# Kernel tuning notes

Measured on AMD Instinct MI355X. Metric: run time of the kernel, lower is better.

## Reference

```python
import jax, jax.numpy as jnp
import numpy as np

DIM = 768
NH = 12
HID = int(DIM * 1.5)  # 1152
B_, T_, W_ = 8, 8, 14
HW = 14 * 14
N = HW + 1
BT = B_ * T_


def _ln(x, g, b, eps=1e-5):
    m = jnp.mean(x, axis=-1, keepdims=True)
    v = jnp.var(x, axis=-1, keepdims=True)
    return (x - m) / jnp.sqrt(v + eps) * g + b


def _attn(x, wqkv, wproj, bproj, nh):
    # manual q@k^T -> softmax -> @v, as in the torch module (no qkv bias)
    b, n, c = x.shape
    hd = c // nh
    scale = hd ** -0.5
    qkv = (x @ wqkv.T).reshape(b, n, 3, nh, hd).transpose(2, 0, 3, 1, 4)
    q, k, v = qkv[0], qkv[1], qkv[2]
    a = jax.nn.softmax(jnp.einsum('bhnd,bhmd->bhnm', q, k) * scale, axis=-1)
    o = jnp.einsum('bhnm,bhmd->bhnd', a, v).transpose(0, 2, 1, 3).reshape(b, n, c)
    return o @ wproj.T + bproj


def setup_inputs() -> dict:
    key = jax.random.key(0)
    ks = jax.random.split(key, 16)
    s = 0.02
    d = {
        'x': jax.random.normal(ks[0], (BT, N, DIM), jnp.float32),
        'ln1_g': jnp.ones((DIM,), jnp.float32),
        'ln1_b': jnp.zeros((DIM,), jnp.float32),
        'qkv_w': jax.random.normal(ks[1], (3 * DIM, DIM), jnp.float32) * s,
        'proj_w': jax.random.normal(ks[2], (DIM, DIM), jnp.float32) * s,
        'proj_b': jnp.zeros((DIM,), jnp.float32),
        'tln_g': jnp.ones((DIM,), jnp.float32),
        'tln_b': jnp.zeros((DIM,), jnp.float32),
        'tqkv_w': jax.random.normal(ks[3], (3 * DIM, DIM), jnp.float32) * s,
        'tproj_w': jax.random.normal(ks[4], (DIM, DIM), jnp.float32) * s,
        'tproj_b': jnp.zeros((DIM,), jnp.float32),
        # module zero-inits temporal_fc; use small random so the branch is exercised
        'tfc_w': jax.random.normal(ks[5], (DIM, DIM), jnp.float32) * s,
        'tfc_b': jnp.zeros((DIM,), jnp.float32),
        'ln2_g': jnp.ones((DIM,), jnp.float32),
        'ln2_b': jnp.zeros((DIM,), jnp.float32),
        'fc1_w': jax.random.normal(ks[6], (HID, DIM), jnp.float32) * s,
        'fc1_b': jnp.zeros((HID,), jnp.float32),
        'fc2_w': jax.random.normal(ks[7], (DIM, HID), jnp.float32) * s,
        'fc2_b': jnp.zeros((DIM,), jnp.float32),
        'B': B_, 'T': T_, 'W': W_,
    }
    return d


def reference(x, ln1_g, ln1_b, qkv_w, proj_w, proj_b,
              tln_g, tln_b, tqkv_w, tproj_w, tproj_b, tfc_w, tfc_b,
              ln2_g, ln2_b, fc1_w, fc1_b, fc2_w, fc2_b, B, T, W):
    bt, n, c = x.shape
    hw = n - 1  # spatial tokens (cls excluded)
    # temporal branch: (b t) hw m -> (b hw) t m
    xt = x[:, 1:, :].reshape(B, T, hw, c).transpose(0, 2, 1, 3).reshape(B * hw, T, c)
    xt = _attn(_ln(xt, tln_g, tln_b), tqkv_w, tproj_w, tproj_b, NH)
    xt = xt.reshape(B, hw, T, c).transpose(0, 2, 1, 3).reshape(bt, hw, c)
    xt = xt @ tfc_w.T + tfc_b
    x = x.at[:, 1:, :].add(xt)  # in-place += in torch
    # spatial attention + residual
    x = x + _attn(_ln(x, ln1_g, ln1_b), qkv_w, proj_w, proj_b, NH)
    # MLP + residual (exact GELU, matching nn.GELU default)
    h = jax.nn.gelu(_ln(x, ln2_g, ln2_b) @ fc1_w.T + fc1_b, approximate=False)
    x = x + (h @ fc2_w.T + fc2_b)
    return x
```

## Files before the change

### kernel.cpp

```cpp
#include <hip/hip_runtime.h>
#include <hip/hip_bf16.h>


#define DIM   768
#define NH    12
#define HD    64
#define HID   1152
#define HIDP  1280
#define B_    8
#define T_    8
#define HW_   196
#define NTOK  197
#define BT_   64
#define MROWS (BT_ * NTOK)
#define TROWS (B_ * HW_ * T_)

typedef __bf16 bf16x8 __attribute__((ext_vector_type(8)));
typedef float  f32x4  __attribute__((ext_vector_type(4)));

__device__ inline float bf2f(ushort u) { return __uint_as_float(((unsigned)u) << 16); }
__device__ inline ushort f2bf(float f) {
    unsigned u = __float_as_uint(f);
    unsigned r = (u + 0x7fffu + ((u >> 16) & 1u)) >> 16;
    return (ushort)r;
}

__device__ inline float wred_sum(float v) {
    #pragma unroll
    for (int m = 32; m; m >>= 1) v += __shfl_xor(v, m);
    return v;
}

__device__ __forceinline__ void gload_lds16(const void* g, void* l) {
    __builtin_amdgcn_global_load_lds(
        (const __attribute__((address_space(1))) unsigned int*)g,
        (__attribute__((address_space(3))) unsigned int*)l, 16, 0, 0);
}

__device__ __forceinline__ int xcd_lin(int gid, int nwg) {
    int q = nwg >> 3, r = nwg & 7;
    int xcd = gid & 7, idx = gid >> 3;
    return (xcd < r ? xcd * (q + 1) : r * (q + 1) + (xcd - r) * q) + idx;
}

#define MFMA16(a, b, c) __builtin_amdgcn_mfma_f32_16x16x32_bf16(a, b, c, 0, 0, 0)

__global__ __launch_bounds__(256) void cast_all(
    const float* s0, ushort* d0, int c0, const float* s1, ushort* d1, int c1,
    const float* s2, ushort* d2, int c2, const float* s3, ushort* d3, int c3,
    const float* s4, ushort* d4, int c4)
{
    int i = blockIdx.x * 256 + threadIdx.x;
    const float* s; ushort* d; int base;
    if      (i < c0) { s = s0; d = d0; base = 0;  }
    else if (i < c1) { s = s1; d = d1; base = c0; }
    else if (i < c2) { s = s2; d = d2; base = c1; }
    else if (i < c3) { s = s3; d = d3; base = c2; }
    else if (i < c4) { s = s4; d = d4; base = c3; }
    else return;
    int k = i - base;
    float4 a = *(const float4*)(s + (size_t)k * 8);
    float4 b = *(const float4*)(s + (size_t)k * 8 + 4);
    ushort o[8] = {f2bf(a.x), f2bf(a.y), f2bf(a.z), f2bf(a.w),
                   f2bf(b.x), f2bf(b.y), f2bf(b.z), f2bf(b.w)};
    *(uint4*)(d + (size_t)k * 8) = *(const uint4*)o;
}

__global__ __launch_bounds__(256) void transpose_cast(const float* __restrict__ in, ushort* __restrict__ out)
{
    __shared__ float t[32][33];
    int bx = blockIdx.x % 24, by = blockIdx.x / 24;
    int lx = threadIdx.x & 31, ly = threadIdx.x >> 5;
    #pragma unroll
    for (int i = 0; i < 32; i += 8)
        t[ly + i][lx] = in[(size_t)(by * 32 + ly + i) * DIM + bx * 32 + lx];
    __syncthreads();
    #pragma unroll
    for (int i = 0; i < 32; i += 8)
        out[(size_t)(bx * 32 + ly + i) * DIM + by * 32 + lx] = f2bf(t[lx][ly + i]);
}

__global__ __launch_bounds__(256) void cast_pad_fc2(const float* __restrict__ in, ushort* __restrict__ out)
{
    int i = blockIdx.x * 256 + threadIdx.x;
    if (i >= DIM * (HIDP / 8)) return;
    int r = i / (HIDP / 8), c8 = (i % (HIDP / 8)) * 8;
    ushort o[8];
    if (c8 < HID) {
        const float* s = in + (size_t)r * HID + c8;
        #pragma unroll
        for (int e = 0; e < 8; ++e) o[e] = f2bf(s[e]);
    } else {
        #pragma unroll
        for (int e = 0; e < 8; ++e) o[e] = 0;
    }
    *(uint4*)(out + (size_t)r * HIDP + c8) = *(const uint4*)o;
}

__global__ __launch_bounds__(256) void pad_bias(const float* __restrict__ in, float* __restrict__ out)
{
    int i = blockIdx.x * 256 + threadIdx.x;
    if (i < HIDP) out[i] = (i < HID) ? in[i] : 0.f;
}

__global__ __launch_bounds__(256) void bias_comb(
    const float* __restrict__ tfc_w, const float* __restrict__ tproj_b,
    const float* __restrict__ tfc_b, float* __restrict__ bc)
{
    int w = blockIdx.x * 4 + (threadIdx.x >> 6);
    int lane = threadIdx.x & 63;
    float s = 0.f;
    for (int j = lane; j < DIM; j += 64) s += tfc_w[(size_t)w * DIM + j] * tproj_b[j];
    s = wred_sum(s);
    if (lane == 0) bc[w] = s + tfc_b[w];
}

__global__ __launch_bounds__(256) void init_cls(const float* __restrict__ x, float* __restrict__ out)
{
    int i = blockIdx.x * 256 + threadIdx.x;
    int r = i / 192, c = (i % 192) * 4;
    size_t off = ((size_t)r * NTOK) * DIM + c;
    *(float4*)(out + off) = *(const float4*)(x + off);
}

enum { EPI_STORE = 0, EPI_BIAS_GELU = 1, EPI_BIAS_ADD = 2, EPI_INIT_TFC = 3 };

template <int KK, int EPI>
__global__ __launch_bounds__(512, 1) void gemm256(
    const ushort* __restrict__ Ag, const ushort* __restrict__ Wg,
    const float* __restrict__ bias, ushort* __restrict__ Cg,
    const float* __restrict__ xsrc, float* __restrict__ xf,
    int M, int N, int nm, int nn, int grp)
{
    __shared__ ushort As[2][256 * 64];
    __shared__ ushort Bs[2][256 * 64];

    const int tid  = threadIdx.x;
    const int lane = tid & 63, wid = tid >> 6;
    const int wr = wid >> 2, wc = wid & 3;
    const int fr = lane & 15, fq = lane >> 4;

    int lin = xcd_lin(blockIdx.x, nm * nn);
    int per = grp * nn;
    int g2 = lin / per, rem = lin % per;
    int bm = g2 * grp;
    int gm = nm - bm; if (gm > grp) gm = grp;
    const int m0 = (bm + rem % gm) * 256;
    const int n0 = (rem / gm) * 256;

    const int srow = wid * 8 + (lane >> 3);
    const int scol = 8 * ((lane & 7) ^ (lane >> 3));
    const ushort* aP[4]; const ushort* bP[4];
    #pragma unroll
    for (int j = 0; j < 4; ++j) {
        int ra = m0 + j * 64 + srow; if (ra >= M) ra = M - 1;
        aP[j] = Ag + (size_t)ra * KK + scol;
        bP[j] = Wg + (size_t)(n0 + j * 64 + srow) * KK + scol;
    }
    const int ldso = (wid * 8) * 64;

    f32x4 acc[8][4] = {};
    bf16x8 af[4][2], b0[2][2], b1[2][2];

    const int sw0 = (fq * 8) ^ ((fr & 7) * 8);
    const int sw1 = (32 + fq * 8) ^ ((fr & 7) * 8);

    #pragma unroll
    for (int j = 0; j < 4; ++j) gload_lds16(aP[j], &As[0][j * 4096 + ldso]);
    #pragma unroll
    for (int j = 0; j < 4; ++j) gload_lds16(bP[j], &Bs[0][j * 4096 + ldso]);

    constexpr int NT = KK / 64;
    #pragma unroll
    for (int t = 0; t < NT; ++t) {
        const int rb = t & 1, wb = rb ^ 1;
        const bool st = (t + 1 < NT);
        const int kw = (t + 1) * 64;

        asm volatile("s_waitcnt vmcnt(0)" ::: "memory");
        __builtin_amdgcn_s_barrier();
        __builtin_amdgcn_sched_barrier(0);

        #pragma unroll
        for (int mf = 0; mf < 4; ++mf) {
            af[mf][0] = *(const bf16x8*)&As[rb][(wr * 128 + mf * 16 + fr) * 64 + sw0];
            af[mf][1] = *(const bf16x8*)&As[rb][(wr * 128 + mf * 16 + fr) * 64 + sw1];
        }
        #pragma unroll
        for (int nf = 0; nf < 2; ++nf) {
            b0[nf][0] = *(const bf16x8*)&Bs[rb][(wc * 64 + nf * 16 + fr) * 64 + sw0];
            b0[nf][1] = *(const bf16x8*)&Bs[rb][(wc * 64 + nf * 16 + fr) * 64 + sw1];
        }
        if (st) {
            #pragma unroll
            for (int j = 0; j < 4; ++j) gload_lds16(aP[j] + kw, &As[wb][j * 4096 + ldso]);
        }
        asm volatile("s_waitcnt lgkmcnt(0)" ::: "memory");
        __builtin_amdgcn_sched_barrier(0);
        __builtin_amdgcn_s_setprio(1);
        #pragma unroll
        for (int mf = 0; mf < 4; ++mf)
            #pragma unroll
            for (int nf = 0; nf < 2; ++nf) {
                acc[mf][nf] = MFMA16(af[mf][0], b0[nf][0], acc[mf][nf]);
                acc[mf][nf] = MFMA16(af[mf][1], b0[nf][1], acc[mf][nf]);
            }
        __builtin_amdgcn_s_setprio(0);
        __builtin_amdgcn_sched_barrier(0);

        #pragma unroll
        for (int nf = 0; nf < 2; ++nf) {
            b1[nf][0] = *(const bf16x8*)&Bs[rb][(wc * 64 + (nf + 2) * 16 + fr) * 64 + sw0];
            b1[nf][1] = *(const bf16x8*)&Bs[rb][(wc * 64 + (nf + 2) * 16 + fr) * 64 + sw1];
        }
        if (st) {
            #pragma unroll
            for (int j = 0; j < 4; ++j) gload_lds16(bP[j] + kw, &Bs[wb][j * 4096 + ldso]);
        }
        asm volatile("s_waitcnt lgkmcnt(0)" ::: "memory");
        __builtin_amdgcn_sched_barrier(0);
        __builtin_amdgcn_s_setprio(1);
        #pragma unroll
        for (int mf = 0; mf < 4; ++mf)
            #pragma unroll
            for (int nf = 0; nf < 2; ++nf) {
                acc[mf][nf + 2] = MFMA16(af[mf][0], b1[nf][0], acc[mf][nf + 2]);
                acc[mf][nf + 2] = MFMA16(af[mf][1], b1[nf][1], acc[mf][nf + 2]);
            }
        __builtin_amdgcn_s_setprio(0);
        __builtin_amdgcn_sched_barrier(0);

        #pragma unroll
        for (int mf = 0; mf < 4; ++mf) {
            af[mf][0] = *(const bf16x8*)&As[rb][(wr * 128 + 64 + mf * 16 + fr) * 64 + sw0];
            af[mf][1] = *(const bf16x8*)&As[rb][(wr * 128 + 64 + mf * 16 + fr) * 64 + sw1];
        }
        asm volatile("s_waitcnt lgkmcnt(0)" ::: "memory");
        __builtin_amdgcn_sched_barrier(0);
        __builtin_amdgcn_s_setprio(1);
        #pragma unroll
        for (int mf = 0; mf < 4; ++mf)
            #pragma unroll
            for (int nf = 0; nf < 2; ++nf) {
                acc[mf + 4][nf] = MFMA16(af[mf][0], b0[nf][0], acc[mf + 4][nf]);
                acc[mf + 4][nf] = MFMA16(af[mf][1], b0[nf][1], acc[mf + 4][nf]);
            }
        __builtin_amdgcn_s_setprio(0);
        __builtin_amdgcn_sched_barrier(0);

        __builtin_amdgcn_s_setprio(1);
        #pragma unroll
        for (int mf = 0; mf < 4; ++mf)
            #pragma unroll
            for (int nf = 0; nf < 2; ++nf) {
                acc[mf + 4][nf + 2] = MFMA16(af[mf][0], b1[nf][0], acc[mf + 4][nf + 2]);
                acc[mf + 4][nf + 2] = MFMA16(af[mf][1], b1[nf][1], acc[mf + 4][nf + 2]);
            }
        __builtin_amdgcn_s_setprio(0);
        __builtin_amdgcn_sched_barrier(0);
    }

    #pragma unroll
    for (int mf = 0; mf < 8; ++mf)
        #pragma unroll
        for (int e = 0; e < 4; ++e) {
            int row = m0 + wr * 128 + mf * 16 + fq * 4 + e;
            if (row >= M) continue;
            size_t dstrow = 0;
            if constexpr (EPI == EPI_INIT_TFC) {
                int t2 = row & 7, pp = (row >> 3) % HW_, bb = row / (HW_ * T_);
                dstrow = ((size_t)(bb * T_ + t2) * NTOK + 1 + pp) * DIM;
            }
            #pragma unroll
            for (int nf = 0; nf < 4; ++nf) {
                int col = n0 + wc * 64 + nf * 16 + fr;
                float v = acc[mf][nf][e];
                if constexpr (EPI != EPI_STORE) v += bias[col];
                if constexpr (EPI == EPI_BIAS_GELU) v = 0.5f * v * (1.0f + erff(v * 0.70710678118654752f));
                if constexpr (EPI == EPI_STORE || EPI == EPI_BIAS_GELU) {
                    Cg[(size_t)row * N + col] = f2bf(v);
                } else if constexpr (EPI == EPI_BIAS_ADD) {
                    xf[(size_t)row * DIM + col] += v;
                } else {
                    xf[dstrow + col] = xsrc[dstrow + col] + v;
                }
            }
        }
}

__global__ __launch_bounds__(256) void ln_f32(
    const float* __restrict__ src, const float* __restrict__ g,
    const float* __restrict__ b, ushort* __restrict__ dst, int rows)
{
    int widx = threadIdx.x >> 6, lane = threadIdx.x & 63;
    int r = blockIdx.x * 4 + widx;
    if (r >= rows) return;
    const float* row = src + (size_t)r * DIM;
    float v[12], sum = 0.f, sq = 0.f;
    #pragma unroll
    for (int c = 0; c < 3; ++c) {
        float4 t = *(const float4*)(row + c * 256 + lane * 4);
        v[c*4+0] = t.x; v[c*4+1] = t.y; v[c*4+2] = t.z; v[c*4+3] = t.w;
        sum += t.x + t.y + t.z + t.w;
        sq  += t.x*t.x + t.y*t.y + t.z*t.z + t.w*t.w;
    }
    sum = wred_sum(sum); sq = wred_sum(sq);
    float mean = sum * (1.f / DIM);
    float var  = sq * (1.f / DIM) - mean * mean;
    float rstd = rsqrtf(var + 1e-5f);
    #pragma unroll
    for (int c = 0; c < 3; ++c) {
        int idx = c * 256 + lane * 4;
        float4 gg = *(const float4*)(g + idx);
        float4 bb = *(const float4*)(b + idx);
        ushort4 o;
        o.x = f2bf((v[c*4+0] - mean) * rstd * gg.x + bb.x);
        o.y = f2bf((v[c*4+1] - mean) * rstd * gg.y + bb.y);
        o.z = f2bf((v[c*4+2] - mean) * rstd * gg.z + bb.z);
        o.w = f2bf((v[c*4+3] - mean) * rstd * gg.w + bb.w);
        *(ushort4*)(dst + (size_t)r * DIM + idx) = o;
    }
}

__global__ __launch_bounds__(256) void ln_gather(
    const float* __restrict__ x, const float* __restrict__ g,
    const float* __restrict__ b, ushort* __restrict__ dst, int rows)
{
    int widx = threadIdx.x >> 6, lane = threadIdx.x & 63;
    int r = blockIdx.x * 4 + widx;
    if (r >= rows) return;
    int t = r & 7, pp = (r >> 3) % HW_, bb = r / (HW_ * T_);
    const float* row = x + ((size_t)(bb * T_ + t) * NTOK + 1 + pp) * DIM;
    float v[12], sum = 0.f, sq = 0.f;
    #pragma unroll
    for (int c = 0; c < 3; ++c) {
        float4 t4 = *(const float4*)(row + c * 256 + lane * 4);
        v[c*4+0] = t4.x; v[c*4+1] = t4.y; v[c*4+2] = t4.z; v[c*4+3] = t4.w;
        sum += t4.x + t4.y + t4.z + t4.w;
        sq  += t4.x*t4.x + t4.y*t4.y + t4.z*t4.z + t4.w*t4.w;
    }
    sum = wred_sum(sum); sq = wred_sum(sq);
    float mean = sum * (1.f / DIM);
    float var  = sq * (1.f / DIM) - mean * mean;
    float rstd = rsqrtf(var + 1e-5f);
    #pragma unroll
    for (int c = 0; c < 3; ++c) {
        int idx = c * 256 + lane * 4;
        float4 gg = *(const float4*)(g + idx);
        float4 bb2 = *(const float4*)(b + idx);
        ushort4 o;
        o.x = f2bf((v[c*4+0] - mean) * rstd * gg.x + bb2.x);
        o.y = f2bf((v[c*4+1] - mean) * rstd * gg.y + bb2.y);
        o.z = f2bf((v[c*4+2] - mean) * rstd * gg.z + bb2.z);
        o.w = f2bf((v[c*4+3] - mean) * rstd * gg.w + bb2.w);
        *(ushort4*)(dst + (size_t)r * DIM + idx) = o;
    }
}

__global__ __launch_bounds__(256) void attn_temporal(
    const ushort* __restrict__ qkv, ushort* __restrict__ O)
{
    int widx = threadIdx.x >> 6, lane = threadIdx.x & 63;
    int w = blockIdx.x * 4 + widx;
    int s = w / NH, h = w % NH;
    int qi = lane >> 3, kj = lane & 7;

    const ushort* qrow = qkv + (size_t)(s * 8 + qi) * (3 * DIM) + h * HD;
    const ushort* krow = qkv + (size_t)(s * 8 + kj) * (3 * DIM) + DIM + h * HD;
    float d = 0.f;
    #pragma unroll
    for (int c = 0; c < 8; ++c) {
        uint4 qa = *(const uint4*)(qrow + c * 8);
        uint4 ka = *(const uint4*)(krow + c * 8);
        const ushort* qs = (const ushort*)&qa;
        const ushort* ks = (const ushort*)&ka;
        #pragma unroll
        for (int e = 0; e < 8; ++e) d += bf2f(qs[e]) * bf2f(ks[e]);
    }
    float sc = d * 0.125f;
    float mx = sc;
    #pragma unroll
    for (int m = 4; m; m >>= 1) mx = fmaxf(mx, __shfl_xor(mx, m));
    float p = expf(sc - mx);
    float sum = p;
    #pragma unroll
    for (int m = 4; m; m >>= 1) sum += __shfl_xor(sum, m);
    p /= sum;

    float o[8] = {};
    int base = lane & ~7;
    #pragma unroll
    for (int t = 0; t < 8; ++t) {
        float pt = __shfl(p, base + t);
        const ushort* vrow = qkv + (size_t)(s * 8 + t) * (3 * DIM) + 2 * DIM + h * HD + kj * 8;
        uint4 va = *(const uint4*)vrow;
        const ushort* vs = (const ushort*)&va;
        #pragma unroll
        for (int e = 0; e < 8; ++e) o[e] += pt * bf2f(vs[e]);
    }
    ushort out[8];
    #pragma unroll
    for (int e = 0; e < 8; ++e) out[e] = f2bf(o[e]);
    *(uint4*)(O + (size_t)(s * 8 + qi) * DIM + h * HD + kj * 8) = *(const uint4*)out;
}

#define KS_STRIDE 72
#define VT_STRIDE 208
#define P_STRIDE  208
#define KS_OFF    0
#define VT_OFF    (197 * KS_STRIDE)
#define P_OFF     (VT_OFF + 64 * VT_STRIDE)
#define LDS_TOT   (P_OFF + 4 * 16 * P_STRIDE)

__global__ __launch_bounds__(256, 2) void attn_spatial_mfma(
    const ushort* __restrict__ qkv, ushort* __restrict__ O)
{
    __shared__ ushort lds[LDS_TOT];
    const int tid = threadIdx.x, lane = tid & 63, wid = tid >> 6;
    const int fr = lane & 15, fq = lane >> 4;
    int lin = xcd_lin(blockIdx.x, BT_ * NH);
    const int s = lin / NH, h = lin % NH;
    const size_t base = (size_t)s * NTOK * (3 * DIM);
    const ushort* Qg = qkv + base + h * HD;
    const ushort* Kg = qkv + base + DIM + h * HD;
    const ushort* Vg = qkv + base + 2 * DIM + h * HD;

    for (int chunk = tid; chunk < NTOK * 8; chunk += 256) {
        int r = chunk >> 3, c = (chunk & 7) * 8;
        uint4 v = *(const uint4*)(Kg + (size_t)r * (3 * DIM) + c);
        *(uint4*)&lds[KS_OFF + r * KS_STRIDE + c] = v;
    }
    for (int chunk = tid; chunk < 208 * 8; chunk += 256) {
        int k = chunk >> 3, c = (chunk & 7) * 8;
        uint4 v = {0u, 0u, 0u, 0u};
        if (k < NTOK) v = *(const uint4*)(Vg + (size_t)k * (3 * DIM) + c);
        const ushort* e = (const ushort*)&v;
        #pragma unroll
        for (int j = 0; j < 8; ++j) lds[VT_OFF + (c + j) * VT_STRIDE + k] = e[j];
    }
    __syncthreads();

    ushort* P = &lds[P_OFF + wid * 16 * P_STRIDE];

    for (int qi = wid; qi < 13; qi += 4) {
        int qrow = qi * 16 + fr; if (qrow > NTOK - 1) qrow = NTOK - 1;
        bf16x8 qf0 = *(const bf16x8*)(Qg + (size_t)qrow * (3 * DIM) + fq * 8);
        bf16x8 qf1 = *(const bf16x8*)(Qg + (size_t)qrow * (3 * DIM) + 32 + fq * 8);

        f32x4 sacc[13];
        #pragma unroll
        for (int t = 0; t < 13; ++t) {
            bf16x8 kf0 = *(const bf16x8*)&lds[KS_OFF + (t * 16 + fr) * KS_STRIDE + fq * 8];
            bf16x8 kf1 = *(const bf16x8*)&lds[KS_OFF + (t * 16 + fr) * KS_STRIDE + 32 + fq * 8];
            f32x4 z = {0.f, 0.f, 0.f, 0.f};
            z = MFMA16(kf0, qf0, z);
            sacc[t] = MFMA16(kf1, qf1, z);
        }

        float m = -1e30f;
        #pragma unroll
        for (int t = 0; t < 13; ++t)
            #pragma unroll
            for (int e = 0; e < 4; ++e) {
                int k = t * 16 + fq * 4 + e;
                float v = (k < NTOK) ? sacc[t][e] * 0.125f : -1e30f;
                sacc[t][e] = v;
                m = fmaxf(m, v);
            }
        m = fmaxf(m, __shfl_xor(m, 16));
        m = fmaxf(m, __shfl_xor(m, 32));
        float sum = 0.f;
        #pragma unroll
        for (int t = 0; t < 13; ++t)
            #pragma unroll
            for (int e = 0; e < 4; ++e) {
                float p = expf(sacc[t][e] - m);
                sacc[t][e] = p;
                sum += p;
            }
        sum += __shfl_xor(sum, 16);
        sum += __shfl_xor(sum, 32);
        float rd = 1.f / sum;

        #pragma unroll
        for (int t = 0; t < 13; ++t) {
            ushort2 w0 = { f2bf(sacc[t][0] * rd), f2bf(sacc[t][1] * rd) };
            ushort2 w1 = { f2bf(sacc[t][2] * rd), f2bf(sacc[t][3] * rd) };
            *(ushort2*)&P[fr * P_STRIDE + t * 16 + fq * 4]     = w0;
            *(ushort2*)&P[fr * P_STRIDE + t * 16 + fq * 4 + 2] = w1;
        }

        f32x4 oacc[4] = {};
        #pragma unroll
        for (int st = 0; st < 6; ++st) {
            bf16x8 pf = *(const bf16x8*)&P[fr * P_STRIDE + st * 32 + fq * 8];
            #pragma unroll
            for (int dt = 0; dt < 4; ++dt) {
                bf16x8 vf = *(const bf16x8*)&lds[VT_OFF + (dt * 16 + fr) * VT_STRIDE + st * 32 + fq * 8];
                oacc[dt] = MFMA16(pf, vf, oacc[dt]);
            }
        }
        {
            bf16x8 zz = {};
            bf16x8 pf = zz;
            if (fq < 2) pf = *(const bf16x8*)&P[fr * P_STRIDE + 192 + fq * 8];
            #pragma unroll
            for (int dt = 0; dt < 4; ++dt) {
                bf16x8 vf = zz;
                if (fq < 2) vf = *(const bf16x8*)&lds[VT_OFF + (dt * 16 + fr) * VT_STRIDE + 192 + fq * 8];
                oacc[dt] = MFMA16(pf, vf, oacc[dt]);
            }
        }

        #pragma unroll
        for (int dt = 0; dt < 4; ++dt)
            #pragma unroll
            for (int e = 0; e < 4; ++e) {
                int q = qi * 16 + fq * 4 + e;
                if (q < NTOK)
                    O[(size_t)(s * NTOK + q) * DIM + h * HD + dt * 16 + fr] = f2bf(oacc[dt][e]);
            }
    }
}

extern "C" void kernel_launch(void* const* d_in, const int* in_sizes, int n_in,
                              void* d_out, int out_size, void* d_ws, size_t ws_size,
                              hipStream_t stream)
{
    const float* x      = (const float*)d_in[0];
    const float* ln1_g  = (const float*)d_in[1];
    const float* ln1_b  = (const float*)d_in[2];
    const float* qkv_w  = (const float*)d_in[3];
    const float* proj_w = (const float*)d_in[4];
    const float* proj_b = (const float*)d_in[5];
    const float* tln_g  = (const float*)d_in[6];
    const float* tln_b  = (const float*)d_in[7];
    const float* tqkv_w = (const float*)d_in[8];
    const float* tproj_w= (const float*)d_in[9];
    const float* tproj_b= (const float*)d_in[10];
    const float* tfc_w  = (const float*)d_in[11];
    const float* tfc_b  = (const float*)d_in[12];
    const float* ln2_g  = (const float*)d_in[13];
    const float* ln2_b  = (const float*)d_in[14];
    const float* fc1_w  = (const float*)d_in[15];
    const float* fc1_b  = (const float*)d_in[16];
    const float* fc2_w  = (const float*)d_in[17];
    const float* fc2_b  = (const float*)d_in[18];

    float* out = (float*)d_out;

    char* p = (char*)d_ws;
    ushort* w_qkv  = (ushort*)p; p += (size_t)(3*DIM*DIM) * 2;
    ushort* w_proj = (ushort*)p; p += (size_t)(DIM*DIM) * 2;
    ushort* w_tqkv = (ushort*)p; p += (size_t)(3*DIM*DIM) * 2;
    ushort* w_tfc  = (ushort*)p; p += (size_t)(DIM*DIM) * 2;
    ushort* tprojT = (ushort*)p; p += (size_t)(DIM*DIM) * 2;
    ushort* w_comb = (ushort*)p; p += (size_t)(DIM*DIM) * 2;
    ushort* w_fc1p = (ushort*)p; p += (size_t)(HIDP*DIM) * 2;
    ushort* w_fc2p = (ushort*)p; p += (size_t)(DIM*HIDP) * 2;
    float*  b_comb = (float*)p;  p += DIM * 4;
    float*  fc1_bp = (float*)p;  p += HIDP * 4;
    ushort* bufA   = (ushort*)p; p += (size_t)MROWS * DIM * 2;
    ushort* bufC   = (ushort*)p; p += (size_t)MROWS * DIM * 2;
    ushort* bufB   = (ushort*)p;

    {
        const int DD8 = DIM * DIM / 8;
        int c0 = 3 * DD8;
        int c1 = c0 + DD8;
        int c2 = c1 + 3 * DD8;
        int c3 = c2 + DD8;
        int c4 = c3 + HID * DIM / 8;
        cast_all<<<dim3((c4 + 255) / 256), dim3(256), 0, stream>>>(
            qkv_w, w_qkv, c0, proj_w, w_proj, c1, tqkv_w, w_tqkv, c2,
            tfc_w, w_tfc, c3, fc1_w, w_fc1p, c4);
    }
    hipMemsetAsync(w_fc1p + (size_t)HID * DIM, 0, (size_t)(HIDP - HID) * DIM * 2, stream);
    transpose_cast<<<dim3(576), dim3(256), 0, stream>>>(tproj_w, tprojT);
    cast_pad_fc2<<<dim3((DIM * (HIDP / 8) + 255) / 256), dim3(256), 0, stream>>>(fc2_w, w_fc2p);
    pad_bias<<<dim3((HIDP + 255) / 256), dim3(256), 0, stream>>>(fc1_b, fc1_bp);
    bias_comb<<<dim3(DIM / 4), dim3(256), 0, stream>>>(tfc_w, tproj_b, tfc_b, b_comb);
    init_cls<<<dim3(48), dim3(256), 0, stream>>>(x, out);

    #define GEMM256(KV, EPI, A, W, BIAS, C, XS, XF, M, N, GRP) \
        gemm256<KV, EPI><<<dim3((((M) + 255) / 256) * ((N) / 256)), dim3(512), 0, stream>>>( \
            A, W, BIAS, C, XS, XF, M, N, ((M) + 255) / 256, (N) / 256, GRP)

    GEMM256(DIM, EPI_STORE, w_tfc, tprojT, nullptr, w_comb, nullptr, nullptr, DIM, DIM, 1);

    ln_gather<<<dim3(TROWS / 4), dim3(256), 0, stream>>>(x, tln_g, tln_b, bufA, TROWS);
    GEMM256(DIM, EPI_STORE, bufA, w_tqkv, nullptr, bufB, nullptr, nullptr, TROWS, 3 * DIM, 1);
    attn_temporal<<<dim3(TROWS * NH / 8 / 4), dim3(256), 0, stream>>>(bufB, bufC);
    GEMM256(DIM, EPI_INIT_TFC, bufC, w_comb, b_comb, nullptr, x, out, TROWS, DIM, 1);

    ln_f32<<<dim3((MROWS + 3) / 4), dim3(256), 0, stream>>>(out, ln1_g, ln1_b, bufA, MROWS);
    GEMM256(DIM, EPI_STORE, bufA, w_qkv, nullptr, bufB, nullptr, nullptr, MROWS, 3 * DIM, 1);
    attn_spatial_mfma<<<dim3(BT_ * NH), dim3(256), 0, stream>>>(bufB, bufC);
    GEMM256(DIM, EPI_BIAS_ADD, bufC, w_proj, proj_b, nullptr, nullptr, out, MROWS, DIM, 1);

    ln_f32<<<dim3((MROWS + 3) / 4), dim3(256), 0, stream>>>(out, ln2_g, ln2_b, bufA, MROWS);
    GEMM256(DIM, EPI_BIAS_GELU, bufA, w_fc1p, fc1_bp, bufB, nullptr, nullptr, MROWS, HIDP, 1);
    GEMM256(HIDP, EPI_BIAS_ADD, bufB, w_fc2p, fc2_b, nullptr, nullptr, out, MROWS, DIM, 1);
    #undef GEMM256
}
```

Before: 412.3 us.

## Switch GEMM main loop to triple-buffered BK=32 LDS pipeline

Reworks the 256x256 GEMM K-loop from double-buffered 64-wide K tiles to three LDS slots of 32-wide K tiles with a prefetch distance of two. A partial vmcnt wait replaces the full drain before each barrier. The goal is to keep global loads in flight across iterations and to simplify fragment loading. In exchange there are twice as many barriers per K. The XOR swizzle on the LDS layout is dropped, which risks bank conflicts on the fragment reads.

```diff
diff --git a/kernel.cpp b/kernel.cpp
--- a/kernel.cpp
+++ b/kernel.cpp
@@ -132,8 +132,8 @@
     const float* __restrict__ xsrc, float* __restrict__ xf,
     int M, int N, int nm, int nn, int grp)
 {
-    __shared__ ushort As[2][256 * 64];
-    __shared__ ushort Bs[2][256 * 64];
+    __shared__ ushort As[3][256 * 32];
+    __shared__ ushort Bs[3][256 * 32];
 
     const int tid  = threadIdx.x;
     const int lane = tid & 63, wid = tid >> 6;
@@ -148,114 +148,72 @@
     const int m0 = (bm + rem % gm) * 256;
     const int n0 = (rem / gm) * 256;
 
-    const int srow = wid * 8 + (lane >> 3);
-    const int scol = 8 * ((lane & 7) ^ (lane >> 3));
-    const ushort* aP[4]; const ushort* bP[4];
-    #pragma unroll
-    for (int j = 0; j < 4; ++j) {
-        int ra = m0 + j * 64 + srow; if (ra >= M) ra = M - 1;
+    const int srow = tid >> 2;
+    const int scol = (tid & 3) * 8;
+    const ushort* aP[2]; const ushort* bP[2];
+    #pragma unroll
+    for (int j = 0; j < 2; ++j) {
+        int ra = m0 + j * 128 + srow; if (ra >= M) ra = M - 1;
         aP[j] = Ag + (size_t)ra * KK + scol;
-        bP[j] = Wg + (size_t)(n0 + j * 64 + srow) * KK + scol;
-    }
-    const int ldso = (wid * 8) * 64;
+        bP[j] = Wg + (size_t)(n0 + j * 128 + srow) * KK + scol;
+    }
+    const int ldso = wid * 512;
+
+    auto STAGE_A = [&](int slot, int k0) {
+        gload_lds16(aP[0] + k0, &As[slot][ldso]);
+        gload_lds16(aP[1] + k0, &As[slot][4096 + ldso]);
+    };
+    auto STAGE_B = [&](int slot, int k0) {
+        gload_lds16(bP[0] + k0, &Bs[slot][ldso]);
+        gload_lds16(bP[1] + k0, &Bs[slot][4096 + ldso]);
+    };
 
     f32x4 acc[8][4] = {};
-    bf16x8 af[4][2], b0[2][2], b1[2][2];
-
-    const int sw0 = (fq * 8) ^ ((fr & 7) * 8);
-    const int sw1 = (32 + fq * 8) ^ ((fr & 7) * 8);
-
-    #pragma unroll
-    for (int j = 0; j < 4; ++j) gload_lds16(aP[j], &As[0][j * 4096 + ldso]);
-    #pragma unroll
-    for (int j = 0; j < 4; ++j) gload_lds16(bP[j], &Bs[0][j * 4096 + ldso]);
-
-    constexpr int NT = KK / 64;
+
+    STAGE_A(0, 0);  STAGE_B(0, 0);
+    STAGE_A(1, 32); STAGE_B(1, 32);
+
+    constexpr int NT = KK / 32;
     #pragma unroll
     for (int t = 0; t < NT; ++t) {
-        const int rb = t & 1, wb = rb ^ 1;
-        const bool st = (t + 1 < NT);
-        const int kw = (t + 1) * 64;
-
-        asm volatile("s_waitcnt vmcnt(0)" ::: "memory");
+        const int sl = t % 3, tg = (t + 2) % 3;
+
+        if (t < NT - 1) asm volatile("s_waitcnt vmcnt(4)" ::: "memory");
+        else            asm volatile("s_waitcnt vmcnt(0)" ::: "memory");
         __builtin_amdgcn_s_barrier();
         __builtin_amdgcn_sched_barrier(0);
 
-        #pragma unroll
-        for (int mf = 0; mf < 4; ++mf) {
-            af[mf][0] = *(const bf16x8*)&As[rb][(wr * 128 + mf * 16 + fr) * 64 + sw0];
-            af[mf][1] = *(const bf16x8*)&As[rb][(wr * 128 + mf * 16 + fr) * 64 + sw1];
-        }
-        #pragma unroll
-        for (int nf = 0; nf < 2; ++nf) {
-            b0[nf][0] = *(const bf16x8*)&Bs[rb][(wc * 64 + nf * 16 + fr) * 64 + sw0];
-            b0[nf][1] = *(const bf16x8*)&Bs[rb][(wc * 64 + nf * 16 + fr) * 64 + sw1];
-        }
-        if (st) {
-            #pragma unroll
-            for (int j = 0; j < 4; ++j) gload_lds16(aP[j] + kw, &As[wb][j * 4096 + ldso]);
-        }
+        bf16x8 a0[4], a1[4], b[4];
+        #pragma unroll
+        for (int mf = 0; mf < 4; ++mf)
+            a0[mf] = *(const bf16x8*)&As[sl][(wr * 128 + mf * 16 + fr) * 32 + fq * 8];
+        #pragma unroll
+        for (int nf = 0; nf < 4; ++nf)
+            b[nf] = *(const bf16x8*)&Bs[sl][(wc * 64 + nf * 16 + fr) * 32 + fq * 8];
+        __builtin_amdgcn_sched_barrier(0);
+        #pragma unroll
+        for (int mf = 0; mf < 4; ++mf)
+            a1[mf] = *(const bf16x8*)&As[sl][(wr * 128 + 64 + mf * 16 + fr) * 32 + fq * 8];
+        if (t + 2 < NT) STAGE_A(tg, (t + 2) * 32);
+        asm volatile("s_waitcnt lgkmcnt(4)" ::: "memory");
+        __builtin_amdgcn_sched_barrier(0);
+        __builtin_amdgcn_s_setprio(1);
+        #pragma unroll
+        for (int mf = 0; mf < 4; ++mf)
+            #pragma unroll
+            for (int nf = 0; nf < 4; ++nf)
+                acc[mf][nf] = MFMA16(a0[mf], b[nf], acc[mf][nf]);
+        __builtin_amdgcn_s_setprio(0);
+        __builtin_amdgcn_sched_barrier(0);
+        if (t + 2 < NT) STAGE_B(tg, (t + 2) * 32);
         asm volatile("s_waitcnt lgkmcnt(0)" ::: "memory");
         __builtin_amdgcn_sched_barrier(0);
         __builtin_amdgcn_s_setprio(1);
         #pragma unroll
         for (int mf = 0; mf < 4; ++mf)
             #pragma unroll
-            for (int nf = 0; nf < 2; ++nf) {
-                acc[mf][nf] = MFMA16(af[mf][0], b0[nf][0], acc[mf][nf]);
-                acc[mf][nf] = MFMA16(af[mf][1], b0[nf][1], acc[mf][nf]);
-            }
-        __builtin_amdgcn_s_setprio(0);
-        __builtin_amdgcn_sched_barrier(0);
-
-        #pragma unroll
-        for (int nf = 0; nf < 2; ++nf) {
-            b1[nf][0] = *(const bf16x8*)&Bs[rb][(wc * 64 + (nf + 2) * 16 + fr) * 64 + sw0];
-            b1[nf][1] = *(const bf16x8*)&Bs[rb][(wc * 64 + (nf + 2) * 16 + fr) * 64 + sw1];
-        }
-        if (st) {
-            #pragma unroll
-            for (int j = 0; j < 4; ++j) gload_lds16(bP[j] + kw, &Bs[wb][j * 4096 + ldso]);
-        }
-        asm volatile("s_waitcnt lgkmcnt(0)" ::: "memory");
-        __builtin_amdgcn_sched_barrier(0);
-        __builtin_amdgcn_s_setprio(1);
-        #pragma unroll
-        for (int mf = 0; mf < 4; ++mf)
-            #pragma unroll
-            for (int nf = 0; nf < 2; ++nf) {
-                acc[mf][nf + 2] = MFMA16(af[mf][0], b1[nf][0], acc[mf][nf + 2]);
-                acc[mf][nf + 2] = MFMA16(af[mf][1], b1[nf][1], acc[mf][nf + 2]);
-            }
-        __builtin_amdgcn_s_setprio(0);
-        __builtin_amdgcn_sched_barrier(0);
-
-        #pragma unroll
-        for (int mf = 0; mf < 4; ++mf) {
-            af[mf][0] = *(const bf16x8*)&As[rb][(wr * 128 + 64 + mf * 16 + fr) * 64 + sw0];
-            af[mf][1] = *(const bf16x8*)&As[rb][(wr * 128 + 64 + mf * 16 + fr) * 64 + sw1];
-        }
-        asm volatile("s_waitcnt lgkmcnt(0)" ::: "memory");
-        __builtin_amdgcn_sched_barrier(0);
-        __builtin_amdgcn_s_setprio(1);
-        #pragma unroll
-        for (int mf = 0; mf < 4; ++mf)
-            #pragma unroll
-            for (int nf = 0; nf < 2; ++nf) {
-                acc[mf + 4][nf] = MFMA16(af[mf][0], b0[nf][0], acc[mf + 4][nf]);
-                acc[mf + 4][nf] = MFMA16(af[mf][1], b0[nf][1], acc[mf + 4][nf]);
-            }
-        __builtin_amdgcn_s_setprio(0);
-        __builtin_amdgcn_sched_barrier(0);
-
-        __builtin_amdgcn_s_setprio(1);
-        #pragma unroll
-        for (int mf = 0; mf < 4; ++mf)
-            #pragma unroll
-            for (int nf = 0; nf < 2; ++nf) {
-                acc[mf + 4][nf + 2] = MFMA16(af[mf][0], b1[nf][0], acc[mf + 4][nf + 2]);
-                acc[mf + 4][nf + 2] = MFMA16(af[mf][1], b1[nf][1], acc[mf + 4][nf + 2]);
-            }
+            for (int nf = 0; nf < 4; ++nf)
+                acc[mf + 4][nf] = MFMA16(a1[mf], b[nf], acc[mf + 4][nf]);
         __builtin_amdgcn_s_setprio(0);
         __builtin_amdgcn_sched_barrier(0);
     }
```

After: 430.3 us. 1.04x slower.

## Restructure 256x256 GEMM into quadrant-split pipeline with half-tile staged loads

Applied to the files above, without the earlier changes.

Reworks the bf16 GEMM main loop so each wave computes four 64x32 quadrants spread across the tile instead of a contiguous 128x64 block. Global-to-LDS loads are split into half-tiles issued up to two k-steps ahead, with partial vmcnt waits and extra barriers between quadrant MFMA phases. This aims to hide load latency and avoid a full drain each iteration. Launch bounds now request two blocks per CU, which caps register use and may cause spills; the finer-grained waits and barriers also risk hazards or extra sync cost.

```diff
diff --git a/kernel.cpp b/kernel.cpp
--- a/kernel.cpp
+++ b/kernel.cpp
@@ -126,7 +126,7 @@
 enum { EPI_STORE = 0, EPI_BIAS_GELU = 1, EPI_BIAS_ADD = 2, EPI_INIT_TFC = 3 };
 
 template <int KK, int EPI>
-__global__ __launch_bounds__(512, 1) void gemm256(
+__global__ __launch_bounds__(512, 2) void gemm256(
     const ushort* __restrict__ Ag, const ushort* __restrict__ Wg,
     const float* __restrict__ bias, ushort* __restrict__ Cg,
     const float* __restrict__ xsrc, float* __restrict__ xf,
@@ -152,140 +152,164 @@
     const int scol = 8 * ((lane & 7) ^ (lane >> 3));
     const ushort* aP[4]; const ushort* bP[4];
     #pragma unroll
-    for (int j = 0; j < 4; ++j) {
-        int ra = m0 + j * 64 + srow; if (ra >= M) ra = M - 1;
-        aP[j] = Ag + (size_t)ra * KK + scol;
-        bP[j] = Wg + (size_t)(n0 + j * 64 + srow) * KK + scol;
-    }
-    const int ldso = (wid * 8) * 64;
-
-    f32x4 acc[8][4] = {};
-    bf16x8 af[4][2], b0[2][2], b1[2][2];
-
-    const int sw0 = (fq * 8) ^ ((fr & 7) * 8);
-    const int sw1 = (32 + fq * 8) ^ ((fr & 7) * 8);
-
-    #pragma unroll
-    for (int j = 0; j < 4; ++j) gload_lds16(aP[j], &As[0][j * 4096 + ldso]);
-    #pragma unroll
-    for (int j = 0; j < 4; ++j) gload_lds16(bP[j], &Bs[0][j * 4096 + ldso]);
+    for (int h = 0; h < 4; ++h) {
+        int ra = m0 + h * 64 + srow; if (ra >= M) ra = M - 1;
+        aP[h] = Ag + (size_t)ra * KK + scol;
+        bP[h] = Wg + (size_t)(n0 + h * 64 + srow) * KK + scol;
+    }
+    const int ldso = wid * 512;
+
+    auto SA = [&](int tt, int hf) {
+        gload_lds16(aP[hf * 2]     + tt * 64, &As[tt & 1][(hf * 128) * 64 + ldso]);
+        gload_lds16(aP[hf * 2 + 1] + tt * 64, &As[tt & 1][(hf * 128 + 64) * 64 + ldso]);
+    };
+    auto SB = [&](int tt, int hf) {
+        gload_lds16(bP[hf * 2]     + tt * 64, &Bs[tt & 1][(hf * 128) * 64 + ldso]);
+        gload_lds16(bP[hf * 2 + 1] + tt * 64, &Bs[tt & 1][(hf * 128 + 64) * 64 + ldso]);
+    };
+
+    f32x4 acc[2][2][4][2] = {};
 
     constexpr int NT = KK / 64;
+    SA(0, 0); SB(0, 0); SB(0, 1); SA(0, 1);
+    if (NT > 1) { SA(1, 0); SB(1, 0); SB(1, 1); }
+    asm volatile("s_waitcnt vmcnt(10)" ::: "memory");
+    __builtin_amdgcn_s_barrier();
+    __builtin_amdgcn_sched_barrier(0);
+
     #pragma unroll
     for (int t = 0; t < NT; ++t) {
-        const int rb = t & 1, wb = rb ^ 1;
-        const bool st = (t + 1 < NT);
-        const int kw = (t + 1) * 64;
-
-        asm volatile("s_waitcnt vmcnt(0)" ::: "memory");
+        const int rb = t & 1;
+        bf16x8 a[4][2], b[2][2][2];
+
+        #pragma unroll
+        for (int mf = 0; mf < 4; ++mf)
+            #pragma unroll
+            for (int ks = 0; ks < 2; ++ks)
+                a[mf][ks] = *(const bf16x8*)&As[rb][(wr * 64 + mf * 16 + fr) * 64 +
+                                                   ((ks * 32 + fq * 8) ^ ((fr & 7) * 8))];
+        #pragma unroll
+        for (int nf = 0; nf < 2; ++nf)
+            #pragma unroll
+            for (int ks = 0; ks < 2; ++ks)
+                b[0][nf][ks] = *(const bf16x8*)&Bs[rb][(wc * 32 + nf * 16 + fr) * 64 +
+                                                      ((ks * 32 + fq * 8) ^ ((fr & 7) * 8))];
+        if (t + 1 < NT) SA(t + 1, 1);
         __builtin_amdgcn_s_barrier();
-        __builtin_amdgcn_sched_barrier(0);
-
-        #pragma unroll
-        for (int mf = 0; mf < 4; ++mf) {
-            af[mf][0] = *(const bf16x8*)&As[rb][(wr * 128 + mf * 16 + fr) * 64 + sw0];
-            af[mf][1] = *(const bf16x8*)&As[rb][(wr * 128 + mf * 16 + fr) * 64 + sw1];
+        asm volatile("s_waitcnt lgkmcnt(0)" ::: "memory");
+        __builtin_amdgcn_sched_barrier(0);
+        __builtin_amdgcn_s_setprio(1);
+        #pragma unroll
+        for (int mf = 0; mf < 4; ++mf)
+            #pragma unroll
+            for (int nf = 0; nf < 2; ++nf) {
+                acc[0][0][mf][nf] = MFMA16(a[mf][0], b[0][nf][0], acc[0][0][mf][nf]);
+                acc[0][0][mf][nf] = MFMA16(a[mf][1], b[0][nf][1], acc[0][0][mf][nf]);
+            }
+        __builtin_amdgcn_s_setprio(0);
+        __builtin_amdgcn_sched_barrier(0);
+        if (t < NT - 1) asm volatile("s_waitcnt vmcnt(10)" ::: "memory");
+        else            asm volatile("s_waitcnt vmcnt(2)"  ::: "memory");
+        __builtin_amdgcn_s_barrier();
+        __builtin_amdgcn_sched_barrier(0);
+
+        #pragma unroll
+        for (int nf = 0; nf < 2; ++nf)
+            #pragma unroll
+            for (int ks = 0; ks < 2; ++ks)
+                b[1][nf][ks] = *(const bf16x8*)&Bs[rb][(128 + wc * 32 + nf * 16 + fr) * 64 +
+                                                      ((ks * 32 + fq * 8) ^ ((fr & 7) * 8))];
+        if (t + 2 < NT) SA(t + 2, 0);
+        __builtin_amdgcn_s_barrier();
+        asm volatile("s_waitcnt lgkmcnt(0)" ::: "memory");
+        __builtin_amdgcn_sched_barrier(0);
+        __builtin_amdgcn_s_setprio(1);
+        #pragma unroll
+        for (int mf = 0; mf < 4; ++mf)
+            #pragma unroll
+            for (int nf = 0; nf < 2; ++nf) {
+                acc[0][1][mf][nf] = MFMA16(a[mf][0], b[1][nf][0], acc[0][1][mf][nf]);
+                acc[0][1][mf][nf] = MFMA16(a[mf][1], b[1][nf][1], acc[0][1][mf][nf]);
+            }
+        __builtin_amdgcn_s_setprio(0);
+        __builtin_amdgcn_sched_barrier(0);
+        if (t < NT - 1) asm volatile("s_waitcnt vmcnt(10)" ::: "memory");
+        else            asm volatile("s_waitcnt vmcnt(0)"  ::: "memory");
+        __builtin_amdgcn_s_barrier();
+        __builtin_amdgcn_sched_barrier(0);
+
+        #pragma unroll
+        for (int mf = 0; mf < 4; ++mf)
+            #pragma unroll
+            for (int ks = 0; ks < 2; ++ks)
+                a[mf][ks] = *(const bf16x8*)&As[rb][(128 + wr * 64 + mf * 16 + fr) * 64 +
+                                                   ((ks * 32 + fq * 8) ^ ((fr & 7) * 8))];
+        if (t + 2 < NT) SB(t + 2, 0);
+        __builtin_amdgcn_s_barrier();
+        asm volatile("s_waitcnt lgkmcnt(0)" ::: "memory");
+        __builtin_amdgcn_sched_barrier(0);
+        __builtin_amdgcn_s_setprio(1);
+        #pragma unroll
+        for (int mf = 0; mf < 4; ++mf)
+            #pragma unroll
+            for (int nf = 0; nf < 2; ++nf) {
+                acc[1][0][mf][nf] = MFMA16(a[mf][0], b[0][nf][0], acc[1][0][mf][nf]);
+                acc[1][0][mf][nf] = MFMA16(a[mf][1], b[0][nf][1], acc[1][0][mf][nf]);
+            }
+        __builtin_amdgcn_s_setprio(0);
+        __builtin_amdgcn_sched_barrier(0);
+        __builtin_amdgcn_s_barrier();
+        __builtin_amdgcn_sched_barrier(0);
+
+        if (t + 2 < NT) SB(t + 2, 1);
+        __builtin_amdgcn_s_setprio(1);
+        #pragma unroll
+        for (int mf = 0; mf < 4; ++mf)
+            #pragma unroll
+            for (int nf = 0; nf < 2; ++nf) {
+                acc[1][1][mf][nf] = MFMA16(a[mf][0], b[1][nf][0], acc[1][1][mf][nf]);
+                acc[1][1][mf][nf] = MFMA16(a[mf][1], b[1][nf][1], acc[1][1][mf][nf]);
+            }
+        __builtin_amdgcn_s_setprio(0);
+        __builtin_amdgcn_sched_barrier(0);
+        if (t + 1 < NT) {
+            if (t + 1 < NT - 1) asm volatile("s_waitcnt vmcnt(10)" ::: "memory");
+            else                asm volatile("s_waitcnt vmcnt(4)"  ::: "memory");
+            __builtin_amdgcn_s_barrier();
+            __builtin_amdgcn_sched_barrier(0);
         }
-        #pragma unroll
-        for (int nf = 0; nf < 2; ++nf) {
-            b0[nf][0] = *(const bf16x8*)&Bs[rb][(wc * 64 + nf * 16 + fr) * 64 + sw0];
-            b0[nf][1] = *(const bf16x8*)&Bs[rb][(wc * 64 + nf * 16 + fr) * 64 + sw1];
-        }
-        if (st) {
-            #pragma unroll
-            for (int j = 0; j < 4; ++j) gload_lds16(aP[j] + kw, &As[wb][j * 4096 + ldso]);
-        }
-        asm volatile("s_waitcnt lgkmcnt(0)" ::: "memory");
-        __builtin_amdgcn_sched_barrier(0);
-        __builtin_amdgcn_s_setprio(1);
+    }
+
+    #pragma unroll
+    for (int qm = 0; qm < 2; ++qm)
         #pragma unroll
         for (int mf = 0; mf < 4; ++mf)
             #pragma unroll
-            for (int nf = 0; nf < 2; ++nf) {
-                acc[mf][nf] = MFMA16(af[mf][0], b0[nf][0], acc[mf][nf]);
-                acc[mf][nf] = MFMA16(af[mf][1], b0[nf][1], acc[mf][nf]);
-            }
-        __builtin_amdgcn_s_setprio(0);
-        __builtin_amdgcn_sched_barrier(0);
-
-        #pragma unroll
-        for (int nf = 0; nf < 2; ++nf) {
-            b1[nf][0] = *(const bf16x8*)&Bs[rb][(wc * 64 + (nf + 2) * 16 + fr) * 64 + sw0];
-            b1[nf][1] = *(const bf16x8*)&Bs[rb][(wc * 64 + (nf + 2) * 16 + fr) * 64 + sw1];
-        }
-        if (st) {
-            #pragma unroll
-            for (int j = 0; j < 4; ++j) gload_lds16(bP[j] + kw, &Bs[wb][j * 4096 + ldso]);
-        }
-        asm volatile("s_waitcnt lgkmcnt(0)" ::: "memory");
-        __builtin_amdgcn_sched_barrier(0);
-        __builtin_amdgcn_s_setprio(1);
-        #pragma unroll
-        for (int mf = 0; mf < 4; ++mf)
-            #pragma unroll
-            for (int nf = 0; nf < 2; ++nf) {
-                acc[mf][nf + 2] = MFMA16(af[mf][0], b1[nf][0], acc[mf][nf + 2]);
-                acc[mf][nf + 2] = MFMA16(af[mf][1], b1[nf][1], acc[mf][nf + 2]);
-            }
-        __builtin_amdgcn_s_setprio(0);
-        __builtin_amdgcn_sched_barrier(0);
-
-        #pragma unroll
-        for (int mf = 0; mf < 4; ++mf) {
-            af[mf][0] = *(const bf16x8*)&As[rb][(wr * 128 + 64 + mf * 16 + fr) * 64 + sw0];
-            af[mf][1] = *(const bf16x8*)&As[rb][(wr * 128 + 64 + mf * 16 + fr) * 64 + sw1];
-        }
-        asm volatile("s_waitcnt lgkmcnt(0)" ::: "memory");
-        __builtin_amdgcn_sched_barrier(0);
-        __builtin_amdgcn_s_setprio(1);
-        #pragma unroll
-        for (int mf = 0; mf < 4; ++mf)
-            #pragma unroll
-            for (int nf = 0; nf < 2; ++nf) {
-                acc[mf + 4][nf] = MFMA16(af[mf][0], b0[nf][0], acc[mf + 4][nf]);
-                acc[mf + 4][nf] = MFMA16(af[mf][1], b0[nf][1], acc[mf + 4][nf]);
-            }
-        __builtin_amdgcn_s_setprio(0);
-        __builtin_amdgcn_sched_barrier(0);
-
-        __builtin_amdgcn_s_setprio(1);
-        #pragma unroll
-        for (int mf = 0; mf < 4; ++mf)
-            #pragma unroll
-            for (int nf = 0; nf < 2; ++nf) {
-                acc[mf + 4][nf + 2] = MFMA16(af[mf][0], b1[nf][0], acc[mf + 4][nf + 2]);
-                acc[mf + 4][nf + 2] = MFMA16(af[mf][1], b1[nf][1], acc[mf + 4][nf + 2]);
-            }
-        __builtin_amdgcn_s_setprio(0);
-        __builtin_amdgcn_sched_barrier(0);
-    }
-
-    #pragma unroll
-    for (int mf = 0; mf < 8; ++mf)
-        #pragma unroll
-        for (int e = 0; e < 4; ++e) {
-            int row = m0 + wr * 128 + mf * 16 + fq * 4 + e;
-            if (row >= M) continue;
-            size_t dstrow = 0;
-            if constexpr (EPI == EPI_INIT_TFC) {
-                int t2 = row & 7, pp = (row >> 3) % HW_, bb = row / (HW_ * T_);
-                dstrow = ((size_t)(bb * T_ + t2) * NTOK + 1 + pp) * DIM;
-            }
-            #pragma unroll
-            for (int nf = 0; nf < 4; ++nf) {
-                int col = n0 + wc * 64 + nf * 16 + fr;
-                float v = acc[mf][nf][e];
-                if constexpr (EPI != EPI_STORE) v += bias[col];
-                if constexpr (EPI == EPI_BIAS_GELU) v = 0.5f * v * (1.0f + erff(v * 0.70710678118654752f));
-                if constexpr (EPI == EPI_STORE || EPI == EPI_BIAS_GELU) {
-                    Cg[(size_t)row * N + col] = f2bf(v);
-                } else if constexpr (EPI == EPI_BIAS_ADD) {
-                    xf[(size_t)row * DIM + col] += v;
-                } else {
-                    xf[dstrow + col] = xsrc[dstrow + col] + v;
+            for (int e = 0; e < 4; ++e) {
+                int row = m0 + qm * 128 + wr * 64 + mf * 16 + fq * 4 + e;
+                if (row >= M) continue;
+                size_t dstrow = 0;
+                if constexpr (EPI == EPI_INIT_TFC) {
+                    int t2 = row & 7, pp = (row >> 3) % HW_, bb = row / (HW_ * T_);
+                    dstrow = ((size_t)(bb * T_ + t2) * NTOK + 1 + pp) * DIM;
                 }
-            }
-        }
+                #pragma unroll
+                for (int qn = 0; qn < 2; ++qn)
+                    #pragma unroll
+                    for (int nf = 0; nf < 2; ++nf) {
+                        int col = n0 + qn * 128 + wc * 32 + nf * 16 + fr;
+                        float v = acc[qm][qn][mf][nf][e];
+                        if constexpr (EPI != EPI_STORE) v += bias[col];
+                        if constexpr (EPI == EPI_BIAS_GELU) v = 0.5f * v * (1.0f + erff(v * 0.70710678118654752f));
+                        if constexpr (EPI == EPI_STORE || EPI == EPI_BIAS_GELU) {
+                            Cg[(size_t)row * N + col] = f2bf(v);
+                        } else if constexpr (EPI == EPI_BIAS_ADD) {
+                            xf[(size_t)row * DIM + col] += v;
+                        } else {
+                            xf[dstrow + col] = xsrc[dstrow + col] + v;
+                        }
+                    }
+            }
 }
 
 __global__ __launch_bounds__(256) void ln_f32(
```

After: 439.7 us. 6.6% more time.
